# Optimization experiments

Hardware: AMD Instinct MI355X
Metric: run time of the kernel (lower is better)

## Reference

```python
import jax, jax.numpy as jnp
import numpy as np

K_NN = 8        # neighbors
RADIUS = 0.1    # neighbor distance cutoff


def setup_inputs() -> dict:
    key = jax.random.key(0)
    k1, k2 = jax.random.split(key)
    B, N, KS = 2, 8192, 16  # batch, points, mask slots
    pc = jax.random.uniform(k1, (B, N, 3), dtype=jnp.float32)
    mask = jax.random.uniform(k2, (B, N, KS), dtype=jnp.float32)
    return {"pc": pc, "mask": mask}


def _knn(k, pc):
    # squared pairwise distances via gemm: (B,N,N)
    sq = jnp.sum(pc * pc, axis=-1)
    d2 = sq[:, :, None] + sq[:, None, :] - 2.0 * jnp.einsum("bnd,bmd->bnm", pc, pc)
    d2 = jnp.maximum(d2, 0.0)
    neg_d2, idx = jax.lax.top_k(-d2, k)          # k smallest distances
    dist = jnp.sqrt(jnp.maximum(-neg_d2, 0.0))   # (B,N,k) euclidean
    return dist, idx


def reference(pc, mask):
    # mask: (B,N,KS) -> (B,KS,N)
    mask_t = jnp.transpose(mask, (0, 2, 1))
    dist, idx = _knn(K_NN, pc)                   # (B,N,k) each
    # replace out-of-radius neighbors with the self index (nearest = self)
    self_idx = idx[:, :, :1]                     # (B,N,1)
    idx = jnp.where(dist > RADIUS, self_idx, idx)
    idx = jax.lax.stop_gradient(idx)
    # grouping_operation: (B,KS,N) gathered at (B,N,k) -> (B,KS,N,k)
    nn_mask = jax.vmap(lambda f, i: f[:, i])(mask_t, idx)
    # loss_norm=1: L1 norm over mask-slot dim (dim=1), mean over k, mean overall
    diff = mask_t[:, :, :, None] - nn_mask       # (B,KS,N,k)
    loss = jnp.sum(jnp.abs(diff), axis=1).mean(axis=-1)  # (B,N)
    return loss.mean()
```

## Files before the change

kernel.cpp:

```cpp
#include <hip/hip_runtime.h>

#define BATCH 2
#define NPTS  8192
#define KS    16
#define KNN   8
#define R2LOOSE 0.0101f
#define KEYMASK 0xFFFFE000u
#define NCELL   1000
#define CSTRIDE 1024

#define QB       64
#define NWAVE    8
#define NTHREADS 512
#define CAP      32
#define SLAB     256
#define NBLK     (BATCH * NPTS / QB)

__device__ __forceinline__ int cell_of(float x, float y, float z) {
    int cx = (int)(x * 10.0f); cx = cx > 9 ? 9 : cx;
    int cy = (int)(y * 10.0f); cy = cy > 9 ? 9 : cy;
    int cz = (int)(z * 10.0f); cz = cz > 9 ? 9 : cz;
    return (cx * 10 + cy) * 10 + cz;
}

__global__ __launch_bounds__(1024) void build_kernel(
    const float* __restrict__ pc,
    float4* __restrict__ cs, int* __restrict__ sidx,
    int* __restrict__ cstart, float* __restrict__ out)
{
    __shared__ int h[1024];
    __shared__ int wsum[16];
    const int blk = blockIdx.x, t = threadIdx.x;
    const int b = blk >> 3, seg = blk & 7;
    const int lane = t & 63, w = t >> 6;

    h[t] = 0;
    if (blk == 0 && t == 0) out[0] = 0.0f;

    const float* p = pc + (size_t)b * NPTS * 3;
    float X[8], Y[8], Z[8]; int CC[8];
#pragma unroll
    for (int j = 0; j < 8; ++j) {
        const int i = j * 1024 + t;
        X[j] = p[3 * i]; Y[j] = p[3 * i + 1]; Z[j] = p[3 * i + 2];
        CC[j] = cell_of(X[j], Y[j], Z[j]);
    }
    __syncthreads();

    int myold = 0;
#pragma unroll
    for (int j = 0; j < 8; ++j) {
        const int old = atomicAdd(&h[CC[j]], 1);
        if (j == seg) myold = old;
        __syncthreads();
    }

    const int sum = h[t];
    int inc = sum;
#pragma unroll
    for (int off = 1; off < 64; off <<= 1) {
        const int v = __shfl_up(inc, off);
        if (lane >= off) inc += v;
    }
    if (lane == 63) wsum[w] = inc;
    __syncthreads();
    if (w == 0) {
        const int v = (lane < 16) ? wsum[lane] : 0;
        int iv = v;
#pragma unroll
        for (int off = 1; off < 16; off <<= 1) {
            const int u = __shfl_up(iv, off);
            if (lane >= off) iv += u;
        }
        if (lane < 16) wsum[lane] = iv - v;
    }
    __syncthreads();
    const int excl = inc - sum + wsum[w];
    if (seg == 0) cstart[b * CSTRIDE + t] = excl;
    __syncthreads();
    h[t] = excl;
    __syncthreads();

    float mx = X[0], my_ = Y[0], mz = Z[0]; int mc = CC[0];
#pragma unroll
    for (int j = 1; j < 8; ++j)
        if (seg == j) { mx = X[j]; my_ = Y[j]; mz = Z[j]; mc = CC[j]; }

    const int pos = h[mc] + myold;
    const float sq = fmaf(mz, mz, fmaf(my_, my_, mx * mx));
    cs[b * NPTS + pos]   = make_float4(mx, my_, mz, -0.5f * sq);
    sidx[b * NPTS + pos] = seg * 1024 + t;
}

#define CEX(a, b) { const unsigned mn_ = min(a, b), mx_ = max(a, b); \
                    a = mn_; b = mx_; }

__global__ __launch_bounds__(512) void knn_loss_kernel(
    const float4* __restrict__ cs,
    const int*    __restrict__ sidx,
    const int*    __restrict__ cstart,
    const float*  __restrict__ mask,
    float* __restrict__ out)
{
    __shared__ float4   stg4[NWAVE][SLAB];
    __shared__ int      stgi[NWAVE][SLAB];
    __shared__ unsigned sbuf[CAP * NTHREADS];
    __shared__ int      fidx[QB * KNN];
    __shared__ int      qid[QB];
    __shared__ float    red[NWAVE];

    const int t = threadIdx.x;
    const int l = t & 63;
    const int k = l & 7;
    const int s = t >> 6;
    const int su = __builtin_amdgcn_readfirstlane(s);
    const int Q = (t >> 3) & 63;
    const int blk = blockIdx.x;
    const int b  = blk >> 7;
    const int q0 = (blk & 127) * QB;
    const int qpos = q0 + Q;

    const float4* csb = cs + b * NPTS;
    const float4 qc = csb[qpos];
    const int    qi = sidx[b * NPTS + qpos];
    if (k == 0) qid[Q] = qi;

    const float qx = qc.x, qy = qc.y, qz = qc.z;
    const float qs = -2.0f * qc.w;
    const float negthr = (qs - R2LOOSE) * 0.5f;
    const unsigned SENT = (__float_as_uint(R2LOOSE) & KEYMASK) | 0x1FFFu;

    int lex = cell_of(qx, qy, qz);
    int cmn = lex, cmx = lex;
#pragma unroll
    for (int off = 32; off; off >>= 1) {
        cmn = min(cmn, __shfl_xor(cmn, off));
        cmx = max(cmx, __shfl_xor(cmx, off));
    }
    const int cfirst = __builtin_amdgcn_readfirstlane(cmn);
    const int clast  = __builtin_amdgcn_readfirstlane(cmx);

    const int* csp = cstart + b * CSTRIDE;
    const int offs[9] = {-110, -100, -90, -10, 0, 10, 90, 100, 110};
    int praw[9], eraw[9];
#pragma unroll
    for (int i = 0; i < 9; ++i) {
        int lo = cfirst + offs[i] - 1;
        int hp = clast + offs[i] + 2;
        lo = min(max(lo, 0), 1000);
        hp = min(max(hp, 0), 1000);
        praw[i] = csp[lo];
        eraw[i] = csp[hp];
    }
    int P[9], cum[9];
    int runv = 0, Cw = 0;
#pragma unroll
    for (int i = 0; i < 9; ++i) {
        const int p = max(praw[i], runv);
        const int e = max(eraw[i], p);
        runv = e;
        P[i] = p; cum[i] = Cw; Cw += e - p;
    }

    int cnt = 0;
    auto EVAL = [&](const float4& c, int spos) {
        const float tt = fmaf(c.x, qx, fmaf(c.y, qy, fmaf(c.z, qz, c.w)));
        const float d2 = fmaxf(fmaf(-2.0f, tt, qs), 0.0f);
        const unsigned key =
            (__float_as_uint(d2) & KEYMASK) | (unsigned)spos;
        const int slot = cnt < (CAP - 1) ? cnt : (CAP - 1);
        sbuf[slot * NTHREADS + t] = key;
        cnt += (tt >= negthr) ? 1 : 0;
    };

    for (int fb = 0; fb < Cw; fb += SLAB) {
        const int n = min(SLAB, Cw - fb);
        for (int f = l; f < n; f += 64) {
            const int g = fb + f;
            int sp = P[0] + g;
#pragma unroll
            for (int i = 1; i < 9; ++i)
                sp = (g >= cum[i]) ? P[i] + (g - cum[i]) : sp;
            stg4[su][f] = csb[sp];
            stgi[su][f] = sp;
        }
        asm volatile("s_waitcnt lgkmcnt(0)" ::: "memory");

        for (int j = k; j < n; j += 8) {
            const float4 c = stg4[su][j];
            const int   sp = stgi[su][j];
            EVAL(c, sp);
        }
        asm volatile("s_waitcnt lgkmcnt(0)" ::: "memory");
    }

    unsigned md[KNN];
#pragma unroll
    for (int kk = 0; kk < KNN; ++kk) md[kk] = SENT;
    const int m = cnt < CAP ? cnt : CAP;
    for (int kk = 0; kk < m; ++kk) {
        unsigned ky = sbuf[kk * NTHREADS + t];
#pragma unroll
        for (int i = 0; i < KNN; ++i) {
            const unsigned mn = min(ky, md[i]);
            const unsigned mx = max(ky, md[i]);
            md[i] = mn; ky = mx;
        }
    }

#pragma unroll
    for (int off = 1; off <= 4; off <<= 1) {
        unsigned bb[8], cc[8];
#pragma unroll
        for (int j = 0; j < 8; ++j)
            bb[j] = (unsigned)__shfl_xor((int)md[j], off);
#pragma unroll
        for (int j = 0; j < 8; ++j)
            cc[j] = min(md[j], bb[7 - j]);
        CEX(cc[0], cc[4]); CEX(cc[1], cc[5]);
        CEX(cc[2], cc[6]); CEX(cc[3], cc[7]);
        CEX(cc[0], cc[2]); CEX(cc[1], cc[3]);
        CEX(cc[4], cc[6]); CEX(cc[5], cc[7]);
        CEX(cc[0], cc[1]); CEX(cc[2], cc[3]);
        CEX(cc[4], cc[5]); CEX(cc[6], cc[7]);
#pragma unroll
        for (int j = 0; j < 8; ++j) md[j] = cc[j];
    }

    {
        const unsigned ky = md[k];
        int nb;
        if (ky >= SENT) {
            nb = qi;
        } else {
            const int sp = (int)(ky & 0x1FFFu);
            const float4 cc2 = csb[sp];
            const float dx = cc2.x - qx;
            const float dy = cc2.y - qy;
            const float dz = cc2.z - qz;
            const float d2 = fmaf(dx, dx, fmaf(dy, dy, dz * dz));
            nb = (sqrtf(d2) > 0.1f) ? qi : sidx[b * NPTS + sp];
        }
        fidx[Q * KNN + k] = nb;
    }
    __syncthreads();

    const int q2 = t >> 3;
    const int j2 = t & 7;
    const int qg = qid[q2];
    const int nb = fidx[q2 * KNN + j2];
    const float* mrow = mask + ((size_t)b * NPTS + qg) * KS;
    const float* nrow = mask + ((size_t)b * NPTS + nb) * KS;
    float acc = 0.0f;
#pragma unroll
    for (int c = 0; c < KS; c += 4) {
        const float4 a = *(const float4*)(mrow + c);
        const float4 v = *(const float4*)(nrow + c);
        acc += fabsf(a.x - v.x) + fabsf(a.y - v.y) +
               fabsf(a.z - v.z) + fabsf(a.w - v.w);
    }

#pragma unroll
    for (int off = 32; off > 0; off >>= 1) acc += __shfl_down(acc, off);
    if ((t & 63) == 0) red[s] = acc;
    __syncthreads();
    if (t == 0) {
        float sum = 0.0f;
#pragma unroll
        for (int i = 0; i < NWAVE; ++i) sum += red[i];
        atomicAdd(out, sum * (1.0f / (BATCH * NPTS * KNN)));
    }
}

extern "C" void kernel_launch(void* const* d_in, const int* in_sizes, int n_in,
                              void* d_out, int out_size, void* d_ws, size_t ws_size,
                              hipStream_t stream) {
    const float* pc   = (const float*)d_in[0];
    const float* mask = (const float*)d_in[1];
    float* out = (float*)d_out;

    float4* cs     = (float4*)d_ws;
    int*    sidx   = (int*)((char*)d_ws + 262144);
    int*    cstart = (int*)((char*)d_ws + 327680);

    hipLaunchKernelGGL(build_kernel, dim3(16), dim3(1024), 0, stream,
                       pc, cs, sidx, cstart, out);
    hipLaunchKernelGGL(knn_loss_kernel, dim3(NBLK), dim3(512), 0, stream,
                       cs, sidx, cstart, mask, out);
}
```

Baseline: 72.18 us.

## Fuse grid build and kNN loss into one cooperative kernel with grid sync

Merges the cell-sort build kernel and the kNN/loss kernel into a single cooperative launch. The first 16 blocks build the spatial grid with 512 threads, each handling two points. A grid-wide sync then separates the build from the query phase. The aim is to remove the second kernel launch and the inter-kernel gap, at the cost of a grid barrier, all 256 blocks having to be co-resident, and higher register pressure in the merged kernel.

```diff
diff --git a/kernel.cpp b/kernel.cpp
--- a/kernel.cpp
+++ b/kernel.cpp
@@ -1,4 +1,7 @@
 #include <hip/hip_runtime.h>
+#include <hip/hip_cooperative_groups.h>
+
+namespace cg = cooperative_groups;
 
 #define BATCH 2
 #define NPTS  8192
@@ -23,84 +26,14 @@
     return (cx * 10 + cy) * 10 + cz;
 }
 
-__global__ __launch_bounds__(1024) void build_kernel(
+#define CEX(a, b) { const unsigned mn_ = min(a, b), mx_ = max(a, b); \
+                    a = mn_; b = mx_; }
+
+__global__ __launch_bounds__(512) void fused_kernel(
     const float* __restrict__ pc,
+    const float* __restrict__ mask,
     float4* __restrict__ cs, int* __restrict__ sidx,
     int* __restrict__ cstart, float* __restrict__ out)
-{
-    __shared__ int h[1024];
-    __shared__ int wsum[16];
-    const int blk = blockIdx.x, t = threadIdx.x;
-    const int b = blk >> 3, seg = blk & 7;
-    const int lane = t & 63, w = t >> 6;
-
-    h[t] = 0;
-    if (blk == 0 && t == 0) out[0] = 0.0f;
-
-    const float* p = pc + (size_t)b * NPTS * 3;
-    float X[8], Y[8], Z[8]; int CC[8];
-#pragma unroll
-    for (int j = 0; j < 8; ++j) {
-        const int i = j * 1024 + t;
-        X[j] = p[3 * i]; Y[j] = p[3 * i + 1]; Z[j] = p[3 * i + 2];
-        CC[j] = cell_of(X[j], Y[j], Z[j]);
-    }
-    __syncthreads();
-
-    int myold = 0;
-#pragma unroll
-    for (int j = 0; j < 8; ++j) {
-        const int old = atomicAdd(&h[CC[j]], 1);
-        if (j == seg) myold = old;
-        __syncthreads();
-    }
-
-    const int sum = h[t];
-    int inc = sum;
-#pragma unroll
-    for (int off = 1; off < 64; off <<= 1) {
-        const int v = __shfl_up(inc, off);
-        if (lane >= off) inc += v;
-    }
-    if (lane == 63) wsum[w] = inc;
-    __syncthreads();
-    if (w == 0) {
-        const int v = (lane < 16) ? wsum[lane] : 0;
-        int iv = v;
-#pragma unroll
-        for (int off = 1; off < 16; off <<= 1) {
-            const int u = __shfl_up(iv, off);
-            if (lane >= off) iv += u;
-        }
-        if (lane < 16) wsum[lane] = iv - v;
-    }
-    __syncthreads();
-    const int excl = inc - sum + wsum[w];
-    if (seg == 0) cstart[b * CSTRIDE + t] = excl;
-    __syncthreads();
-    h[t] = excl;
-    __syncthreads();
-
-    float mx = X[0], my_ = Y[0], mz = Z[0]; int mc = CC[0];
-#pragma unroll
-    for (int j = 1; j < 8; ++j)
-        if (seg == j) { mx = X[j]; my_ = Y[j]; mz = Z[j]; mc = CC[j]; }
-
-    const int pos = h[mc] + myold;
-    const float sq = fmaf(mz, mz, fmaf(my_, my_, mx * mx));
-    cs[b * NPTS + pos]   = make_float4(mx, my_, mz, -0.5f * sq);
-    sidx[b * NPTS + pos] = seg * 1024 + t;
-}
-
-#define CEX(a, b) { const unsigned mn_ = min(a, b), mx_ = max(a, b); \
-                    a = mn_; b = mx_; }
-
-__global__ __launch_bounds__(512) void knn_loss_kernel(
-    const float4* __restrict__ cs,
-    const int*    __restrict__ sidx,
-    const int*    __restrict__ cstart,
-    const float*  __restrict__ mask,
-    float* __restrict__ out)
 {
     __shared__ float4   stg4[NWAVE][SLAB];
     __shared__ int      stgi[NWAVE][SLAB];
@@ -108,14 +41,100 @@
     __shared__ int      fidx[QB * KNN];
     __shared__ int      qid[QB];
     __shared__ float    red[NWAVE];
+    __shared__ int      h[1024];
+    __shared__ int      wsum[8];
 
     const int t = threadIdx.x;
+    const int blk = blockIdx.x;
+    const int lane = t & 63;
+    const int w = t >> 6;
+
+    if (blk < 16) {
+        const int bb = blk >> 3, seg = blk & 7;
+        h[t] = 0; h[t + 512] = 0;
+        if (blk == 0 && t == 0) out[0] = 0.0f;
+
+        const float* p = pc + (size_t)bb * NPTS * 3;
+        float X0[8], Y0[8], Z0[8], X1[8], Y1[8], Z1[8];
+        int C0[8], C1[8];
+#pragma unroll
+        for (int j = 0; j < 8; ++j) {
+            const int i0 = j * 1024 + t;
+            const int i1 = i0 + 512;
+            X0[j] = p[3 * i0]; Y0[j] = p[3 * i0 + 1]; Z0[j] = p[3 * i0 + 2];
+            X1[j] = p[3 * i1]; Y1[j] = p[3 * i1 + 1]; Z1[j] = p[3 * i1 + 2];
+            C0[j] = cell_of(X0[j], Y0[j], Z0[j]);
+            C1[j] = cell_of(X1[j], Y1[j], Z1[j]);
+        }
+        __syncthreads();
+
+        int r0 = 0, r1 = 0;
+#pragma unroll
+        for (int j = 0; j < 8; ++j) {
+            const int o0 = atomicAdd(&h[C0[j]], 1);
+            const int o1 = atomicAdd(&h[C1[j]], 1);
+            if (j == seg) { r0 = o0; r1 = o1; }
+            __syncthreads();
+        }
+
+        const int c0 = h[2 * t], c1 = h[2 * t + 1];
+        const int ps = c0 + c1;
+        int inc = ps;
+#pragma unroll
+        for (int off = 1; off < 64; off <<= 1) {
+            const int v = __shfl_up(inc, off);
+            if (lane >= off) inc += v;
+        }
+        if (lane == 63) wsum[w] = inc;
+        __syncthreads();
+        if (w == 0) {
+            const int v = (lane < 8) ? wsum[lane] : 0;
+            int iv = v;
+#pragma unroll
+            for (int off = 1; off < 8; off <<= 1) {
+                const int u = __shfl_up(iv, off);
+                if (lane >= off) iv += u;
+            }
+            if (lane < 8) wsum[lane] = iv - v;
+        }
+        __syncthreads();
+        const int excl = inc - ps + wsum[w];
+        const int s0 = excl, s1 = excl + c0;
+        if (seg == 0) {
+            cstart[bb * CSTRIDE + 2 * t]     = s0;
+            cstart[bb * CSTRIDE + 2 * t + 1] = s1;
+        }
+        __syncthreads();
+        h[2 * t] = s0; h[2 * t + 1] = s1;
+        __syncthreads();
+
+        float ax = X0[0], ay = Y0[0], az = Z0[0]; int ac = C0[0];
+        float bx = X1[0], by = Y1[0], bz = Z1[0]; int bc = C1[0];
+#pragma unroll
+        for (int j = 1; j < 8; ++j)
+            if (seg == j) {
+                ax = X0[j]; ay = Y0[j]; az = Z0[j]; ac = C0[j];
+                bx = X1[j]; by = Y1[j]; bz = Z1[j]; bc = C1[j];
+            }
+
+        const int pos0 = h[ac] + r0;
+        const int pos1 = h[bc] + r1;
+        const float sqa = fmaf(az, az, fmaf(ay, ay, ax * ax));
+        const float sqb = fmaf(bz, bz, fmaf(by, by, bx * bx));
+        cs[bb * NPTS + pos0]   = make_float4(ax, ay, az, -0.5f * sqa);
+        cs[bb * NPTS + pos1]   = make_float4(bx, by, bz, -0.5f * sqb);
+        sidx[bb * NPTS + pos0] = seg * 1024 + t;
+        sidx[bb * NPTS + pos1] = seg * 1024 + 512 + t;
+        __threadfence();
+    }
+
+    cg::this_grid().sync();
+
     const int l = t & 63;
     const int k = l & 7;
     const int s = t >> 6;
     const int su = __builtin_amdgcn_readfirstlane(s);
     const int Q = (t >> 3) & 63;
-    const int blk = blockIdx.x;
     const int b  = blk >> 7;
     const int q0 = (blk & 127) * QB;
     const int qpos = q0 + Q;
@@ -210,13 +229,13 @@
 
 #pragma unroll
     for (int off = 1; off <= 4; off <<= 1) {
-        unsigned bb[8], cc[8];
+        unsigned bb2[8], cc[8];
 #pragma unroll
         for (int j = 0; j < 8; ++j)
-            bb[j] = (unsigned)__shfl_xor((int)md[j], off);
+            bb2[j] = (unsigned)__shfl_xor((int)md[j], off);
 #pragma unroll
         for (int j = 0; j < 8; ++j)
-            cc[j] = min(md[j], bb[7 - j]);
+            cc[j] = min(md[j], bb2[7 - j]);
         CEX(cc[0], cc[4]); CEX(cc[1], cc[5]);
         CEX(cc[2], cc[6]); CEX(cc[3], cc[7]);
         CEX(cc[0], cc[2]); CEX(cc[1], cc[3]);
@@ -283,8 +302,8 @@
     int*    sidx   = (int*)((char*)d_ws + 262144);
     int*    cstart = (int*)((char*)d_ws + 327680);
 
-    hipLaunchKernelGGL(build_kernel, dim3(16), dim3(1024), 0, stream,
-                       pc, cs, sidx, cstart, out);
-    hipLaunchKernelGGL(knn_loss_kernel, dim3(NBLK), dim3(512), 0, stream,
-                       cs, sidx, cstart, mask, out);
+    void* args[] = {(void*)&pc, (void*)&mask, (void*)&cs,
+                    (void*)&sidx, (void*)&cstart, (void*)&out};
+    hipLaunchCooperativeKernel((const void*)fused_kernel,
+                               dim3(NBLK), dim3(NTHREADS), args, 0, stream);
 }
```

New measurement: 110.2 us. +52.6%, slower.
